# Kernel tuning notes

Hardware: AMD Instinct MI355X
Metric: run time of the kernel (lower is better)

Reference implementation:

```python
import jax, jax.numpy as jnp
import numpy as np

N_NODES = 50000
N_EDGES = 400000
NODE_FEAT = 32
HIDDEN = 256
ACTION_DIM = 6
NUM_GRAPHS = 64


def setup_inputs() -> dict:
    key = jax.random.key(0)
    ks = jax.random.split(key, 9)
    x = jax.random.normal(ks[0], (N_NODES, NODE_FEAT), dtype=jnp.float32)
    edge_index = jax.random.randint(ks[1], (2, N_EDGES), 0, N_NODES, dtype=jnp.int32)
    batch = jnp.sort(jax.random.randint(ks[2], (N_NODES,), 0, NUM_GRAPHS, dtype=jnp.int32))
    # GCNConv weights (PyG stores Linear without bias + separate bias term;
    # here W is [in, out] so h = x @ W)
    s1 = 1.0 / np.sqrt(NODE_FEAT)
    s2 = 1.0 / np.sqrt(HIDDEN)
    W1 = jax.random.uniform(ks[3], (NODE_FEAT, HIDDEN), jnp.float32, -s1, s1)
    b1 = jnp.zeros((HIDDEN,), jnp.float32)
    W2 = jax.random.uniform(ks[4], (HIDDEN, HIDDEN), jnp.float32, -s2, s2)
    b2 = jnp.zeros((HIDDEN,), jnp.float32)
    Wf = jax.random.uniform(ks[5], (HIDDEN, 2 * ACTION_DIM), jnp.float32, -s2, s2)
    bf = jax.random.uniform(ks[6], (2 * ACTION_DIM,), jnp.float32, -s2, s2)
    return {"x": x, "edge_index": edge_index, "batch": batch,
            "W1": W1, "b1": b1, "W2": W2, "b2": b2, "Wf": Wf, "bf": bf}


def gcn_conv(x, src, dst, deg_inv_sqrt, W, b, num_nodes):
    # PyG GCNConv: h = x @ W, messages h[src] * norm scattered to dst, + bias.
    h = x @ W  # [N, out]
    norm = deg_inv_sqrt[src] * deg_inv_sqrt[dst]  # [E+N]
    msgs = h[src] * norm[:, None]  # [E+N, out]  (dominant memory traffic)
    out = jax.ops.segment_sum(msgs, dst, num_segments=num_nodes)
    return out + b


def reference(x, edge_index, batch, W1, b1, W2, b2, Wf, bf):
    num_nodes = x.shape[0]
    loop = jnp.arange(num_nodes, dtype=edge_index.dtype)
    src = jnp.concatenate([edge_index[0], loop])  # self-loops, PyG default
    dst = jnp.concatenate([edge_index[1], loop])
    deg = jax.ops.segment_sum(jnp.ones_like(dst, dtype=x.dtype), dst,
                              num_segments=num_nodes)  # >=1 due to self-loops
    deg_inv_sqrt = jax.lax.rsqrt(deg)

    h = jax.nn.relu(gcn_conv(x, src, dst, deg_inv_sqrt, W1, b1, num_nodes))
    h = jax.nn.relu(gcn_conv(h, src, dst, deg_inv_sqrt, W2, b2, num_nodes))

    # global_mean_pool over graph ids
    sums = jax.ops.segment_sum(h, batch, num_segments=NUM_GRAPHS)
    counts = jax.ops.segment_sum(jnp.ones((num_nodes,), x.dtype), batch,
                                 num_segments=NUM_GRAPHS)
    pooled = sums / jnp.maximum(counts, 1.0)[:, None]  # [G, HIDDEN]

    mls = pooled @ Wf + bf  # [G, 2*ACTION_DIM]
    mean, log_std = jnp.split(mls, 2, axis=-1)
    std = jnp.exp(jnp.clip(log_std, -20.0, 2.0))
    return mean, std
```

## Files before the change

### kernel.cpp

```cpp
#include <hip/hip_runtime.h>
#include <math.h>

#define NN 50000
#define FEAT 32
#define HID 256
#define NGRAPH 64
#define CAP 48

typedef __attribute__((ext_vector_type(8))) short bfrag;
typedef __attribute__((ext_vector_type(8))) unsigned short u16x8;
typedef __attribute__((ext_vector_type(4))) float f32x4;

__device__ __forceinline__ float bf2f(unsigned short u) {
    union { unsigned int i; float f; } v; v.i = ((unsigned int)u) << 16; return v.f;
}
__device__ __forceinline__ unsigned short f2bf(float f) {
    union { float f; unsigned int i; } v; v.f = f;
    unsigned int r = v.i + 0x7fffu + ((v.i >> 16) & 1u);
    return (unsigned short)(r >> 16);
}

__device__ __forceinline__ void pack_w(const float* __restrict__ W,
                                       unsigned short* __restrict__ Wp, int K, int o) {
    int j    = o & 7;
    int lane = (o >> 3) & 63;
    int rest = o >> 9;
    int nst  = K >> 5;
    int ks   = rest & (nst - 1);
    int nb   = rest / nst;
    int n = nb * 16 + (lane & 15);
    int k = ks * 32 + (lane >> 4) * 8 + j;
    Wp[o] = f2bf(W[(size_t)k * HID + n]);
}

__global__ void k_prep(float4* __restrict__ zp, int n16,
                       const float* __restrict__ W1, const float* __restrict__ W2,
                       unsigned short* __restrict__ W1p, unsigned short* __restrict__ W2p) {
    int i = blockIdx.x * blockDim.x + threadIdx.x;
    if (i < n16) zp[i] = make_float4(0.f, 0.f, 0.f, 0.f);
    if (i < FEAT * HID) pack_w(W1, W1p, FEAT, i);
    int o2 = i - FEAT * HID;
    if (o2 >= 0 && o2 < HID * HID) pack_w(W2, W2p, HID, o2);
}

__global__ void k_setup(const int* __restrict__ src, const int* __restrict__ dst,
                        const int* __restrict__ batch,
                        int* __restrict__ counter, unsigned short* __restrict__ csr,
                        int* __restrict__ starts, int E, int N) {
    int e = blockIdx.x * blockDim.x + threadIdx.x;
    if (e < E) {
        int d = dst[e];
        int p = atomicAdd(&counter[d], 1);
        if (p < CAP) csr[(size_t)d * CAP + p] = (unsigned short)src[e];
    }
    if (e < N) {
        int b = batch[e];
        int prev = (e == 0) ? -1 : batch[e - 1];
        if (b != prev) {
            for (int g = prev + 1; g <= b; ++g) starts[g] = e;
        }
        if (e == N - 1) {
            for (int g = b + 1; g <= NGRAPH; ++g) starts[g] = N;
        }
    }
}

__global__ void k_aggx(const float* __restrict__ x, const int* __restrict__ cnt,
                       const unsigned short* __restrict__ csr,
                       unsigned short* __restrict__ out, int N) {
    int node = blockIdx.x * 8 + (threadIdx.x >> 5);
    if (node >= N) return;
    int col = threadIdx.x & 31;
    int ecnt = cnt[node];
    float dn = rsqrtf((float)(ecnt + 1));
    int e = ecnt > CAP ? CAP : ecnt;
    const unsigned short* lst = &csr[(size_t)node * CAP];

    float acc = x[(size_t)node * FEAT + col] * dn;
    int i = 0;
    for (; i + 8 <= e; i += 8) {
        u16x8 s = *(const u16x8*)&lst[i];
        float vs[8];
#pragma unroll
        for (int j = 0; j < 8; ++j) {
            int sj = (int)s[j];
            vs[j] = x[(size_t)sj * FEAT + col] * rsqrtf((float)(cnt[sj] + 1));
        }
        acc += ((vs[0] + vs[1]) + (vs[2] + vs[3])) + ((vs[4] + vs[5]) + (vs[6] + vs[7]));
    }
    for (; i + 4 <= e; i += 4) {
        float vs[4];
#pragma unroll
        for (int j = 0; j < 4; ++j) {
            int sj = (int)lst[i + j];
            vs[j] = x[(size_t)sj * FEAT + col] * rsqrtf((float)(cnt[sj] + 1));
        }
        acc += (vs[0] + vs[1]) + (vs[2] + vs[3]);
    }
    for (; i < e; ++i) {
        int sj = (int)lst[i];
        acc += x[(size_t)sj * FEAT + col] * rsqrtf((float)(cnt[sj] + 1));
    }
    out[(size_t)node * FEAT + col] = f2bf(acc * dn);
}

__global__ void k_aggh(const unsigned short* __restrict__ h, const int* __restrict__ cnt,
                       const unsigned short* __restrict__ csr,
                       unsigned short* __restrict__ out, int N) {
    int gw = (int)((blockIdx.x * (size_t)blockDim.x + threadIdx.x) >> 6);
    int lane = threadIdx.x & 63;
    int node = gw * 2 + (lane >> 5);
    if (node >= N) return;
    int c0 = (lane & 31) * 8;

    int ecnt = cnt[node];
    float dn = rsqrtf((float)(ecnt + 1));
    int e = ecnt > CAP ? CAP : ecnt;
    const unsigned short* lst = &csr[(size_t)node * CAP];

    bfrag sv = *(const bfrag*)&h[(size_t)node * HID + c0];
    float a[8];
#pragma unroll
    for (int j = 0; j < 8; ++j) a[j] = bf2f((unsigned short)sv[j]);

    int i = 0;
    for (; i + 8 <= e; i += 8) {
        u16x8 s = *(const u16x8*)&lst[i];
        bfrag w0 = *(const bfrag*)&h[(size_t)s[0] * HID + c0];
        bfrag w1 = *(const bfrag*)&h[(size_t)s[1] * HID + c0];
        bfrag w2 = *(const bfrag*)&h[(size_t)s[2] * HID + c0];
        bfrag w3 = *(const bfrag*)&h[(size_t)s[3] * HID + c0];
        bfrag w4 = *(const bfrag*)&h[(size_t)s[4] * HID + c0];
        bfrag w5 = *(const bfrag*)&h[(size_t)s[5] * HID + c0];
        bfrag w6 = *(const bfrag*)&h[(size_t)s[6] * HID + c0];
        bfrag w7 = *(const bfrag*)&h[(size_t)s[7] * HID + c0];
#pragma unroll
        for (int j = 0; j < 8; ++j) {
            a[j] += ((bf2f((unsigned short)w0[j]) + bf2f((unsigned short)w1[j]))
                   + (bf2f((unsigned short)w2[j]) + bf2f((unsigned short)w3[j])))
                  + ((bf2f((unsigned short)w4[j]) + bf2f((unsigned short)w5[j]))
                   + (bf2f((unsigned short)w6[j]) + bf2f((unsigned short)w7[j])));
        }
    }
    for (; i + 4 <= e; i += 4) {
        bfrag w0 = *(const bfrag*)&h[(size_t)lst[i]     * HID + c0];
        bfrag w1 = *(const bfrag*)&h[(size_t)lst[i + 1] * HID + c0];
        bfrag w2 = *(const bfrag*)&h[(size_t)lst[i + 2] * HID + c0];
        bfrag w3 = *(const bfrag*)&h[(size_t)lst[i + 3] * HID + c0];
#pragma unroll
        for (int j = 0; j < 8; ++j)
            a[j] += (bf2f((unsigned short)w0[j]) + bf2f((unsigned short)w1[j]))
                  + (bf2f((unsigned short)w2[j]) + bf2f((unsigned short)w3[j]));
    }
    for (; i < e; ++i) {
        bfrag w = *(const bfrag*)&h[(size_t)lst[i] * HID + c0];
#pragma unroll
        for (int j = 0; j < 8; ++j) a[j] += bf2f((unsigned short)w[j]);
    }
    bfrag o;
#pragma unroll
    for (int j = 0; j < 8; ++j) o[j] = (short)f2bf(a[j] * dn);
    *(bfrag*)&out[(size_t)node * HID + c0] = o;
}

__global__ __launch_bounds__(256, 4)
void k_mmf(const unsigned short* __restrict__ A, const unsigned short* __restrict__ Wp,
           const float* __restrict__ bias, const int* __restrict__ cnt,
           unsigned short* __restrict__ C, int M) {
    __shared__ unsigned short lds[64 * 264];
    const int K = FEAT;
    int tid  = threadIdx.x;
    int lane = tid & 63;
    int wid  = tid >> 6;
    int l15  = lane & 15;
    int lq   = lane >> 4;
    int row0 = blockIdx.x * 64;

    const int P = K + 8;
    {
        int flat = tid * 8;
        int row = flat >> 5;
        int col = flat & 31;
        bfrag v = {0, 0, 0, 0, 0, 0, 0, 0};
        int gr = row0 + row;
        if (gr < M) v = *(const bfrag*)&A[(size_t)gr * K + col];
        *(bfrag*)&lds[row * P + col] = v;
    }
    __syncthreads();

    f32x4 acc[4][4];
#pragma unroll
    for (int mi = 0; mi < 4; ++mi)
#pragma unroll
        for (int ni = 0; ni < 4; ++ni) acc[mi][ni] = (f32x4){0.f, 0.f, 0.f, 0.f};

    bfrag fb[4];
#pragma unroll
    for (int ni = 0; ni < 4; ++ni) {
        size_t off = (((size_t)(wid * 4 + ni)) * 64 + lane) * 8;
        fb[ni] = *(const bfrag*)&Wp[off];
    }
    bfrag fa[4];
#pragma unroll
    for (int mi = 0; mi < 4; ++mi)
        fa[mi] = *(const bfrag*)&lds[(mi * 16 + l15) * P + lq * 8];
#pragma unroll
    for (int mi = 0; mi < 4; ++mi)
#pragma unroll
        for (int ni = 0; ni < 4; ++ni)
            acc[mi][ni] = __builtin_amdgcn_mfma_f32_16x16x32_bf16(fb[ni], fa[mi], acc[mi][ni], 0, 0, 0);

    float4 bv[4];
#pragma unroll
    for (int ni = 0; ni < 4; ++ni)
        bv[ni] = *(const float4*)&bias[(wid * 4 + ni) * 16 + lq * 4];
    float sv[4];
#pragma unroll
    for (int mi = 0; mi < 4; ++mi) {
        int gr = row0 + mi * 16 + l15;
        sv[mi] = (gr < M) ? rsqrtf((float)(cnt[gr] + 1)) : 0.f;
    }

    __syncthreads();
#pragma unroll
    for (int mi = 0; mi < 4; ++mi) {
#pragma unroll
        for (int ni = 0; ni < 4; ++ni) {
            const float* bp = (const float*)&bv[ni];
            ushort4 o;
            o.x = f2bf(fmaxf(acc[mi][ni][0] + bp[0], 0.f) * sv[mi]);
            o.y = f2bf(fmaxf(acc[mi][ni][1] + bp[1], 0.f) * sv[mi]);
            o.z = f2bf(fmaxf(acc[mi][ni][2] + bp[2], 0.f) * sv[mi]);
            o.w = f2bf(fmaxf(acc[mi][ni][3] + bp[3], 0.f) * sv[mi]);
            *(ushort4*)&lds[(mi * 16 + l15) * 264 + (wid * 4 + ni) * 16 + lq * 4] = o;
        }
    }
    __syncthreads();

#pragma unroll
    for (int i = 0; i < 8; ++i) {
        int F = (i * 256 + tid) * 8;
        int row = F >> 8;
        int col = F & 255;
        int gr = row0 + row;
        if (gr < M) {
            bfrag v = *(const bfrag*)&lds[row * 264 + col];
            *(bfrag*)&C[(size_t)gr * HID + col] = v;
        }
    }
}

__global__ __launch_bounds__(256, 4)
void k_mmfp(const unsigned short* __restrict__ A, const unsigned short* __restrict__ Wp,
            const float* __restrict__ bias, const int* __restrict__ batch,
            float* __restrict__ pooled, int M) {
    __shared__ unsigned short lds[64 * 264];
    __shared__ int bshare[64];
    const int K = HID;
    int tid  = threadIdx.x;
    int lane = tid & 63;
    int wid  = tid >> 6;
    int l15  = lane & 15;
    int lq   = lane >> 4;
    int row0 = blockIdx.x * 64;

    if (tid < 64) {
        int gr = row0 + tid;
        bshare[tid] = (gr < M) ? batch[gr] : -1;
    }

    const int P = K + 8;
    for (int it = 0; it < 8; ++it) {
        int flat = (it * 256 + tid) * 8;
        int row = flat >> 8;
        int col = flat & 255;
        bfrag v = {0, 0, 0, 0, 0, 0, 0, 0};
        int gr = row0 + row;
        if (gr < M) v = *(const bfrag*)&A[(size_t)gr * K + col];
        *(bfrag*)&lds[row * P + col] = v;
    }
    __syncthreads();

    f32x4 acc[4][4];
#pragma unroll
    for (int mi = 0; mi < 4; ++mi)
#pragma unroll
        for (int ni = 0; ni < 4; ++ni) acc[mi][ni] = (f32x4){0.f, 0.f, 0.f, 0.f};

    for (int ks = 0; ks < 8; ++ks) {
        bfrag fb[4];
#pragma unroll
        for (int ni = 0; ni < 4; ++ni) {
            size_t off = (((size_t)(wid * 4 + ni) * 8 + ks) * 64 + lane) * 8;
            fb[ni] = *(const bfrag*)&Wp[off];
        }
        bfrag fa[4];
        int koff = ks * 32 + lq * 8;
#pragma unroll
        for (int mi = 0; mi < 4; ++mi)
            fa[mi] = *(const bfrag*)&lds[(mi * 16 + l15) * P + koff];
#pragma unroll
        for (int mi = 0; mi < 4; ++mi)
#pragma unroll
            for (int ni = 0; ni < 4; ++ni)
                acc[mi][ni] = __builtin_amdgcn_mfma_f32_16x16x32_bf16(fb[ni], fa[mi], acc[mi][ni], 0, 0, 0);
    }

    float4 bv[4];
#pragma unroll
    for (int ni = 0; ni < 4; ++ni)
        bv[ni] = *(const float4*)&bias[(wid * 4 + ni) * 16 + lq * 4];

    __syncthreads();
#pragma unroll
    for (int mi = 0; mi < 4; ++mi) {
#pragma unroll
        for (int ni = 0; ni < 4; ++ni) {
            const float* bp = (const float*)&bv[ni];
            ushort4 o;
            o.x = f2bf(fmaxf(acc[mi][ni][0] + bp[0], 0.f));
            o.y = f2bf(fmaxf(acc[mi][ni][1] + bp[1], 0.f));
            o.z = f2bf(fmaxf(acc[mi][ni][2] + bp[2], 0.f));
            o.w = f2bf(fmaxf(acc[mi][ni][3] + bp[3], 0.f));
            *(ushort4*)&lds[(mi * 16 + l15) * 264 + (wid * 4 + ni) * 16 + lq * 4] = o;
        }
    }
    __syncthreads();

    int c = tid;
    float pacc = 0.f;
    int cur = bshare[0];
    for (int r = 0; r < 64; ++r) {
        int g = bshare[r];
        if (g != cur) {
            if (cur >= 0) atomicAdd(&pooled[(size_t)cur * HID + c], pacc);
            pacc = 0.f; cur = g;
        }
        pacc += bf2f(lds[r * 264 + c]);
    }
    if (cur >= 0) atomicAdd(&pooled[(size_t)cur * HID + c], pacc);
}

__global__ void k_head(const float* __restrict__ pooled, const int* __restrict__ starts,
                       const float* __restrict__ Wf, const float* __restrict__ bf,
                       float* __restrict__ out) {
    int t = blockIdx.x * blockDim.x + threadIdx.x;
    if (t >= NGRAPH * 12) return;
    int g = t / 12, j = t % 12;
    float cntf = (float)(starts[g + 1] - starts[g]);
    float inv = 1.f / fmaxf(cntf, 1.f);
    float s = 0.f;
    for (int k = 0; k < HID; ++k) s += pooled[(size_t)g * HID + k] * Wf[k * 12 + j];
    s = s * inv + bf[j];
    if (j < 6) {
        out[g * 6 + j] = s;
    } else {
        float ls = fminf(fmaxf(s, -20.f), 2.f);
        out[NGRAPH * 6 + g * 6 + (j - 6)] = expf(ls);
    }
}

extern "C" void kernel_launch(void* const* d_in, const int* in_sizes, int n_in,
                              void* d_out, int out_size, void* d_ws, size_t ws_size,
                              hipStream_t stream) {
    const float* x     = (const float*)d_in[0];
    const int*   ei    = (const int*)d_in[1];
    const int*   batch = (const int*)d_in[2];
    const float* W1    = (const float*)d_in[3];
    const float* b1    = (const float*)d_in[4];
    const float* W2    = (const float*)d_in[5];
    const float* b2    = (const float*)d_in[6];
    const float* Wf    = (const float*)d_in[7];
    const float* bfv   = (const float*)d_in[8];
    float* out = (float*)d_out;

    const int E = in_sizes[1] / 2;
    const int N = in_sizes[2];
    const int* srcp = ei;
    const int* dstp = ei + E;

    char* ws = (char*)d_ws;
    const size_t OFF_CTR    = 0;
    const size_t OFF_POOLED = 200192;
    const size_t ZERO_BYTES = 265728;
    const size_t OFF_STARTS = 265728;
    const size_t OFF_W1P    = 266240;
    const size_t OFF_W2P    = 282624;
    const size_t OFF_CSR    = 413696;
    const size_t OFF_AGGX   = 5213696;
    const size_t OFF_H1     = 8413696;
    const size_t OFF_G      = 34013696;

    int*            ctr    = (int*)(ws + OFF_CTR);
    float*          pooled = (float*)(ws + OFF_POOLED);
    int*            starts = (int*)(ws + OFF_STARTS);
    unsigned short* W1p    = (unsigned short*)(ws + OFF_W1P);
    unsigned short* W2p    = (unsigned short*)(ws + OFF_W2P);
    unsigned short* csr    = (unsigned short*)(ws + OFF_CSR);
    unsigned short* aggX   = (unsigned short*)(ws + OFF_AGGX);
    unsigned short* h1     = (unsigned short*)(ws + OFF_H1);
    unsigned short* g      = (unsigned short*)(ws + OFF_G);

    const int T = 256;
    const int prep_n = (FEAT + HID) * HID;
    k_prep<<<(prep_n + T - 1) / T, T, 0, stream>>>((float4*)ws, 265728 / 16, W1, W2, W1p, W2p);
    k_setup<<<(E + T - 1) / T, T, 0, stream>>>(srcp, dstp, batch, ctr, csr, starts, E, N);

    k_aggx<<<(N + 7) / 8, T, 0, stream>>>(x, ctr, csr, aggX, N);
    k_mmf<<<(N + 63) / 64, T, 0, stream>>>(aggX, W1p, b1, ctr, h1, N);

    k_aggh<<<(N + 7) / 8, T, 0, stream>>>(h1, ctr, csr, g, N);
    k_mmfp<<<(N + 63) / 64, T, 0, stream>>>(g, W2p, b2, batch, pooled, N);

    k_head<<<3, T, 0, stream>>>(pooled, starts, Wf, bfv, out);
}
```

Baseline: 121.2 us.

## Store hidden features in 32-column panels to localize gather traffic

The layer-1 output and aggregated layer-2 input now use a panel-major layout: eight panels of 32 bf16 columns, each holding all nodes contiguously. The aggregation kernel gives each block one panel and 64 nodes, so the gathers in a given phase touch a 3.2 MB panel that is more likely to stay in cache than the full 25 MB feature matrix. The matmul store and the layer-2 load index into the panel layout to match. In exchange, each gathered row is only 64 bytes, and the same CSR list is read eight times.

New measurement: 117.3 us. -3.2%, faster.

```diff
diff --git a/kernel.cpp b/kernel.cpp
--- a/kernel.cpp
+++ b/kernel.cpp
@@ -104,21 +104,22 @@
     out[(size_t)node * FEAT + col] = f2bf(acc * dn);
 }
 
-__global__ void k_aggh(const unsigned short* __restrict__ h, const int* __restrict__ cnt,
+__global__ void k_aggh(const unsigned short* __restrict__ hp, const int* __restrict__ cnt,
                        const unsigned short* __restrict__ csr,
-                       unsigned short* __restrict__ out, int N) {
-    int gw = (int)((blockIdx.x * (size_t)blockDim.x + threadIdx.x) >> 6);
-    int lane = threadIdx.x & 63;
-    int node = gw * 2 + (lane >> 5);
+                       unsigned short* __restrict__ outp, int N) {
+    int panel = blockIdx.x & 7;
+    int node = (blockIdx.x >> 3) * 64 + (threadIdx.x >> 2);
     if (node >= N) return;
-    int c0 = (lane & 31) * 8;
+    int c0 = (threadIdx.x & 3) * 8;
+    const unsigned short* h = hp + (size_t)panel * N * 32;
+    unsigned short* out = outp + (size_t)panel * N * 32;
 
     int ecnt = cnt[node];
     float dn = rsqrtf((float)(ecnt + 1));
     int e = ecnt > CAP ? CAP : ecnt;
     const unsigned short* lst = &csr[(size_t)node * CAP];
 
-    bfrag sv = *(const bfrag*)&h[(size_t)node * HID + c0];
+    bfrag sv = *(const bfrag*)&h[(size_t)node * 32 + c0];
     float a[8];
 #pragma unroll
     for (int j = 0; j < 8; ++j) a[j] = bf2f((unsigned short)sv[j]);
@@ -126,14 +127,14 @@
     int i = 0;
     for (; i + 8 <= e; i += 8) {
         u16x8 s = *(const u16x8*)&lst[i];
-        bfrag w0 = *(const bfrag*)&h[(size_t)s[0] * HID + c0];
-        bfrag w1 = *(const bfrag*)&h[(size_t)s[1] * HID + c0];
-        bfrag w2 = *(const bfrag*)&h[(size_t)s[2] * HID + c0];
-        bfrag w3 = *(const bfrag*)&h[(size_t)s[3] * HID + c0];
-        bfrag w4 = *(const bfrag*)&h[(size_t)s[4] * HID + c0];
-        bfrag w5 = *(const bfrag*)&h[(size_t)s[5] * HID + c0];
-        bfrag w6 = *(const bfrag*)&h[(size_t)s[6] * HID + c0];
-        bfrag w7 = *(const bfrag*)&h[(size_t)s[7] * HID + c0];
+        bfrag w0 = *(const bfrag*)&h[(size_t)s[0] * 32 + c0];
+        bfrag w1 = *(const bfrag*)&h[(size_t)s[1] * 32 + c0];
+        bfrag w2 = *(const bfrag*)&h[(size_t)s[2] * 32 + c0];
+        bfrag w3 = *(const bfrag*)&h[(size_t)s[3] * 32 + c0];
+        bfrag w4 = *(const bfrag*)&h[(size_t)s[4] * 32 + c0];
+        bfrag w5 = *(const bfrag*)&h[(size_t)s[5] * 32 + c0];
+        bfrag w6 = *(const bfrag*)&h[(size_t)s[6] * 32 + c0];
+        bfrag w7 = *(const bfrag*)&h[(size_t)s[7] * 32 + c0];
 #pragma unroll
         for (int j = 0; j < 8; ++j) {
             a[j] += ((bf2f((unsigned short)w0[j]) + bf2f((unsigned short)w1[j]))
@@ -143,24 +144,24 @@
         }
     }
     for (; i + 4 <= e; i += 4) {
-        bfrag w0 = *(const bfrag*)&h[(size_t)lst[i]     * HID + c0];
-        bfrag w1 = *(const bfrag*)&h[(size_t)lst[i + 1] * HID + c0];
-        bfrag w2 = *(const bfrag*)&h[(size_t)lst[i + 2] * HID + c0];
-        bfrag w3 = *(const bfrag*)&h[(size_t)lst[i + 3] * HID + c0];
+        bfrag w0 = *(const bfrag*)&h[(size_t)lst[i]     * 32 + c0];
+        bfrag w1 = *(const bfrag*)&h[(size_t)lst[i + 1] * 32 + c0];
+        bfrag w2 = *(const bfrag*)&h[(size_t)lst[i + 2] * 32 + c0];
+        bfrag w3 = *(const bfrag*)&h[(size_t)lst[i + 3] * 32 + c0];
 #pragma unroll
         for (int j = 0; j < 8; ++j)
             a[j] += (bf2f((unsigned short)w0[j]) + bf2f((unsigned short)w1[j]))
                   + (bf2f((unsigned short)w2[j]) + bf2f((unsigned short)w3[j]));
     }
     for (; i < e; ++i) {
-        bfrag w = *(const bfrag*)&h[(size_t)lst[i] * HID + c0];
+        bfrag w = *(const bfrag*)&h[(size_t)lst[i] * 32 + c0];
 #pragma unroll
         for (int j = 0; j < 8; ++j) a[j] += bf2f((unsigned short)w[j]);
     }
     bfrag o;
 #pragma unroll
     for (int j = 0; j < 8; ++j) o[j] = (short)f2bf(a[j] * dn);
-    *(bfrag*)&out[(size_t)node * HID + c0] = o;
+    *(bfrag*)&out[(size_t)node * 32 + c0] = o;
 }
 
 __global__ __launch_bounds__(256, 4)
@@ -245,7 +246,7 @@
         int gr = row0 + row;
         if (gr < M) {
             bfrag v = *(const bfrag*)&lds[row * 264 + col];
-            *(bfrag*)&C[(size_t)gr * HID + col] = v;
+            *(bfrag*)&C[((size_t)(col >> 5) * M + gr) * 32 + (col & 31)] = v;
         }
     }
 }
@@ -276,7 +277,7 @@
         int col = flat & 255;
         bfrag v = {0, 0, 0, 0, 0, 0, 0, 0};
         int gr = row0 + row;
-        if (gr < M) v = *(const bfrag*)&A[(size_t)gr * K + col];
+        if (gr < M) v = *(const bfrag*)&A[((size_t)(col >> 5) * M + gr) * 32 + (col & 31)];
         *(bfrag*)&lds[row * P + col] = v;
     }
     __syncthreads();
@@ -382,7 +383,6 @@
     char* ws = (char*)d_ws;
     const size_t OFF_CTR    = 0;
     const size_t OFF_POOLED = 200192;
-    const size_t ZERO_BYTES = 265728;
     const size_t OFF_STARTS = 265728;
     const size_t OFF_W1P    = 266240;
     const size_t OFF_W2P    = 282624;
@@ -409,7 +409,7 @@
     k_aggx<<<(N + 7) / 8, T, 0, stream>>>(x, ctr, csr, aggX, N);
     k_mmf<<<(N + 63) / 64, T, 0, stream>>>(aggX, W1p, b1, ctr, h1, N);
 
-    k_aggh<<<(N + 7) / 8, T, 0, stream>>>(h1, ctr, csr, g, N);
+    k_aggh<<<((N + 63) / 64) * 8, T, 0, stream>>>(h1, ctr, csr, g, N);
     k_mmfp<<<(N + 63) / 64, T, 0, stream>>>(g, W2p, b2, batch, pooled, N);
 
     k_head<<<3, T, 0, stream>>>(pooled, starts, Wf, bfv, out);
```
